# Kernel tuning notes

Hardware: AMD Instinct MI355X
Metric: run time of the kernel (lower is better)

## Reference

```python
import jax, jax.numpy as jnp
import numpy as np

B, T, M, E, H, D = 4, 1024, 1024, 1024, 16, 64
SCALE = D ** (-0.5)


def setup_inputs() -> dict:
    key = jax.random.key(0)
    ks = jax.random.split(key, 8)
    w = 0.02  # weight scale for numerical stability of softmax
    return {
        "x": jax.random.normal(ks[0], (B, T, E), jnp.float32),
        "xl_memory": jax.random.normal(ks[1], (B, M, 2, H * D), jnp.float32),
        "relative_positions": jax.random.normal(ks[2], (H, T, M + T), jnp.float32),
        "Wq": jax.random.normal(ks[3], (E, H * D), jnp.float32) * w,
        "bq": jnp.zeros((H * D,), jnp.float32),
        "Wk": jax.random.normal(ks[4], (E, H * D), jnp.float32) * w,
        "bk": jnp.zeros((H * D,), jnp.float32),
        "Wv": jax.random.normal(ks[5], (E, H * D), jnp.float32) * w,
        "bv": jnp.zeros((H * D,), jnp.float32),
        "Wo": jax.random.normal(ks[6], (H * D, E), jnp.float32) * w,
        "bo": jnp.zeros((E,), jnp.float32),
    }


def reference(x, xl_memory, relative_positions, Wq, bq, Wk, bk, Wv, bv, Wo, bo):
    b, t, _ = x.shape
    q = (x @ Wq + bq) * SCALE                     # [b, t, H*D] (scale applied to queries)
    k = x @ Wk + bk
    v = x @ Wv + bv
    k_xl = xl_memory[:, :, 0]                      # [b, m, H*D]
    v_xl = xl_memory[:, :, 1]
    m = k_xl.shape[1]
    keys = jnp.concatenate((k_xl, k), axis=1)      # [b, j, H*D], j = m + t
    values = jnp.concatenate((v_xl, v), axis=1)
    j = keys.shape[1]

    qh = q.reshape(b, t, H, D).transpose(0, 2, 1, 3)       # b h i d
    kh = keys.reshape(b, j, H, D).transpose(0, 2, 1, 3)    # b h j d
    vh = values.reshape(b, j, H, D).transpose(0, 2, 1, 3)  # b h j d

    qk = jnp.einsum("bhid,bhjd->bhij", qh, kh)
    qk = relative_positions[..., -t:, -j:] + qk
    qk = qk * SCALE                                # second scale, faithful to source
    mask = jnp.triu(jnp.ones((t, j), dtype=bool), j - t + 1)
    qk = jnp.where(mask, -jnp.inf, qk)
    attn = jax.nn.softmax(qk, axis=-1)             # dropout p=0.0 -> identity

    qkv = jnp.einsum("bhij,bhjd->bhid", attn, vh)
    qkv = qkv.transpose(0, 2, 1, 3).reshape(b, t, H * D)
    out = qkv @ Wo + bo

    kv_memories = jnp.stack((keys, values), axis=-2)  # [b, j, 2, H*D]
    kv_to_add_xl = kv_memories[:, -m:]                 # [b, m, 2, H*D]
    return out, kv_to_add_xl
```

## Files before the change

### kernel.cpp

```cpp
#include <hip/hip_runtime.h>
#include <hip/hip_bf16.h>

typedef unsigned short u16;
typedef unsigned int u32;
typedef __attribute__((ext_vector_type(8))) short short8;
typedef __attribute__((ext_vector_type(4))) float f32x4;

#define B_ 4
#define T_ 1024
#define E_ 1024
#define NH 16
#define HD 1024
#define JTOT 2048
#define SCALE 0.125f
#define LOG2E 1.44269504f

__device__ __forceinline__ u16 f2b(float f) {
  u32 x = __float_as_uint(f);
  u32 r = (x + 0x7fffu + ((x >> 16) & 1u)) >> 16;
  return (u16)r;
}
__device__ __forceinline__ u16 f2b_fast(float f) {
  return (u16)((__float_as_uint(f) + 0x8000u) >> 16);
}
__device__ __forceinline__ float b2f(u16 b) {
  return __uint_as_float((u32)b << 16);
}
__device__ __forceinline__ float fexp2(float x) {
  float r;
  asm("v_exp_f32 %0, %1" : "=v"(r) : "v"(x));
  return r;
}
__device__ __forceinline__ u32 cvtpk(float lo, float hi) {
  u32 r;
  asm("v_cvt_pk_bf16_f32 %0, %1, %2" : "=v"(r) : "v"(lo), "v"(hi));
  return r;
}

__device__ __forceinline__ void gload_lds16(const void* g, void* l) {
  __builtin_amdgcn_global_load_lds((const __attribute__((address_space(1))) u32*)g,
                                   (__attribute__((address_space(3))) u32*)l, 16, 0, 0);
}

__device__ __forceinline__ short8 pack8(float4 f0, float4 f1) {
  short8 o;
  o[0] = (short)f2b(f0.x); o[1] = (short)f2b(f0.y);
  o[2] = (short)f2b(f0.z); o[3] = (short)f2b(f0.w);
  o[4] = (short)f2b(f1.x); o[5] = (short)f2b(f1.y);
  o[6] = (short)f2b(f1.z); o[7] = (short)f2b(f1.w);
  return o;
}

__global__ __launch_bounds__(256) void cvt_all(
    const float* __restrict__ x, const float* __restrict__ Wq, const float* __restrict__ Wk,
    const float* __restrict__ Wv, const float* __restrict__ Wo, const float* __restrict__ xl,
    u16* __restrict__ xb, u16* __restrict__ wqkvT, u16* __restrict__ woT,
    u16* __restrict__ kt, u16* __restrict__ vt) {
  int bx = blockIdx.x;
  if (bx < 2048) {
    int i = bx * 256 + threadIdx.x;
    const float4* p = (const float4*)x + (size_t)i * 2;
    ((short8*)xb)[i] = pack8(p[0], p[1]);
  } else if (bx < 3072) {
    __shared__ float tile[64][65];
    int idx = bx - 2048;
    int z = idx >> 8, yy = (idx >> 4) & 15, xx = idx & 15;
    const float* W;
    u16* WT;
    if (z == 0) { W = Wq; WT = wqkvT; }
    else if (z == 1) { W = Wk; WT = wqkvT + (size_t)1024 * 1024; }
    else if (z == 2) { W = Wv; WT = wqkvT + (size_t)2048 * 1024; }
    else { W = Wo; WT = woT; }
    int t = threadIdx.x;
    int r0 = yy * 64, c0 = xx * 64;
#pragma unroll
    for (int i = 0; i < 16; ++i) {
      int r = i * 4 + (t >> 6), c = t & 63;
      tile[r][c] = W[(size_t)(r0 + r) * 1024 + c0 + c];
    }
    __syncthreads();
#pragma unroll
    for (int i = 0; i < 16; ++i) {
      int r = i * 4 + (t >> 6), c = t & 63;
      WT[(size_t)(c0 + r) * 1024 + r0 + c] = f2b(tile[c][r]);
    }
  } else if (bx < 5120) {
    int i = (bx - 3072) * 256 + threadIdx.x;
    int hd8 = i & 127, j = (i >> 7) & 1023, b = i >> 17;
    const float4* p = (const float4*)(xl + ((((size_t)b * 1024 + j) * 2 + 0) * 1024 + (size_t)hd8 * 8));
    short8 o = pack8(p[0], p[1]);
    int h = hd8 >> 3, d0 = (hd8 & 7) * 8;
    int jc = j >> 6, jl = j & 63;
    u16* dst = kt + (((size_t)(b * 16 + h) * 32 + jc) * 4096) + jl * 64 + (d0 ^ ((jl & 7) << 3));
    *(short8*)dst = o;
  } else {
    __shared__ u16 Vl[64 * 72];
    int bxx = bx - 5120;
    int jc = bxx & 15, h = (bxx >> 4) & 15, b = bxx >> 8;
    int t = threadIdx.x;
    int j0 = jc * 64;
#pragma unroll
    for (int it = 0; it < 2; ++it) {
      int p = t + 256 * it;
      int j = p >> 3, d8 = p & 7;
      const float4* src = (const float4*)(xl + ((((size_t)b * 1024 + j0 + j) * 2 + 1) * 1024 + h * 64 + (size_t)d8 * 8));
      *(short8*)&Vl[j * 72 + d8 * 8] = pack8(src[0], src[1]);
    }
    __syncthreads();
#pragma unroll
    for (int it = 0; it < 2; ++it) {
      int p = t + 256 * it;
      int d = p >> 3, j8 = p & 7;
      short8 o;
#pragma unroll
      for (int e = 0; e < 8; ++e) o[e] = (short)Vl[(j8 * 8 + e) * 72 + d];
      u16* dst = vt + (((size_t)(b * 16 + h) * 32 + jc) * 4096) + d * 64 + ((j8 * 8) ^ ((d & 7) << 3));
      *(short8*)dst = o;
    }
  }
}

__global__ __launch_bounds__(256) void gemm_qkv(
    const u16* __restrict__ A, const u16* __restrict__ BT,
    const float* __restrict__ b0, const float* __restrict__ b1, const float* __restrict__ b2,
    u16* __restrict__ qb, u16* __restrict__ kbp, u16* __restrict__ vb) {
  __shared__ __align__(16) u16 As[128 * 32];
  __shared__ __align__(16) u16 Bs[128 * 32];
  const int t = threadIdx.x;
  const int lane = t & 63, wv = t >> 6;
  const int wr = wv >> 1, wc = wv & 1;
  const int xcd = blockIdx.x & 7, loc = blockIdx.x >> 3;
  const int m0 = (loc / 3) * 128;
  const int n0 = (xcd * 3 + loc % 3) * 128;
  const int lr = lane & 15, lg = lane >> 4;

  f32x4 acc[4][4] = {};

  for (int kc = 0; kc < 1024; kc += 32) {
    __syncthreads();
#pragma unroll
    for (int i = 0; i < 2; ++i) {
      int p = t + 256 * i;
      gload_lds16(A + (size_t)(m0 + (p >> 2)) * 1024 + kc + (p & 3) * 8, &As[p * 8]);
    }
#pragma unroll
    for (int i = 0; i < 2; ++i) {
      int p = t + 256 * i;
      gload_lds16(BT + (size_t)(n0 + (p >> 2)) * 1024 + kc + (p & 3) * 8, &Bs[p * 8]);
    }
    __syncthreads();

    short8 af[4], bf[4];
#pragma unroll
    for (int mf = 0; mf < 4; ++mf)
      af[mf] = *(const short8*)&As[(wr * 64 + mf * 16 + lr) * 32 + lg * 8];
#pragma unroll
    for (int nf = 0; nf < 4; ++nf)
      bf[nf] = *(const short8*)&Bs[(wc * 64 + nf * 16 + lr) * 32 + lg * 8];
#pragma unroll
    for (int mf = 0; mf < 4; ++mf)
#pragma unroll
      for (int nf = 0; nf < 4; ++nf)
        acc[mf][nf] = __builtin_amdgcn_mfma_f32_16x16x32_bf16(af[mf], bf[nf], acc[mf][nf], 0, 0, 0);
  }

#pragma unroll
  for (int mf = 0; mf < 4; ++mf) {
#pragma unroll
    for (int nf = 0; nf < 4; ++nf) {
#pragma unroll
      for (int r = 0; r < 4; ++r) {
        int row = m0 + wr * 64 + mf * 16 + lg * 4 + r;
        int col = n0 + wc * 64 + nf * 16 + lr;
        float v = acc[mf][nf][r];
        int b = row >> 10, tt = row & 1023;
        if (col < 1024) {
          qb[(size_t)row * HD + col] = f2b((v + b0[col]) * (SCALE * SCALE * LOG2E));
        } else if (col < 2048) {
          int hd = col - 1024;
          kbp[(size_t)(b * 1024 + tt) * 1024 + hd] = f2b(v + b1[hd]);
        } else {
          int hd = col - 2048;
          vb[(size_t)(b * 1024 + tt) * 1024 + hd] = f2b(v + b2[hd]);
        }
      }
    }
  }
}

__global__ __launch_bounds__(256) void post_gemm(const u16* __restrict__ kbp, const u16* __restrict__ vbp,
                                                 float* __restrict__ kvout, u16* __restrict__ kt,
                                                 u16* __restrict__ vt) {
  int bx = blockIdx.x;
  if (bx < 2048) {
    int i = bx * 256 + threadIdx.x;
    int hd8 = i & 127, tt = (i >> 7) & 1023, b = i >> 17;
    size_t src = ((size_t)(b * 1024 + tt)) * 1024 + (size_t)hd8 * 8;
    short8 k8 = *(const short8*)&kbp[src];
    short8 v8 = *(const short8*)&vbp[src];
    float4 k0, k1, v0, v1;
#pragma unroll
    for (int e = 0; e < 4; ++e) {
      ((float*)&k0)[e] = b2f((u16)k8[e]); ((float*)&k1)[e] = b2f((u16)k8[e + 4]);
      ((float*)&v0)[e] = b2f((u16)v8[e]); ((float*)&v1)[e] = b2f((u16)v8[e + 4]);
    }
    float* kdst = kvout + (((size_t)(b * 1024 + tt) * 2 + 0) * 1024) + hd8 * 8;
    float* vdst = kvout + (((size_t)(b * 1024 + tt) * 2 + 1) * 1024) + hd8 * 8;
    ((float4*)kdst)[0] = k0; ((float4*)kdst)[1] = k1;
    ((float4*)vdst)[0] = v0; ((float4*)vdst)[1] = v1;
    int h = hd8 >> 3, d0 = (hd8 & 7) * 8;
    int jc = 16 + (tt >> 6), jl = tt & 63;
    u16* ktdst = kt + (((size_t)(b * 16 + h) * 32 + jc) * 4096) + jl * 64 + (d0 ^ ((jl & 7) << 3));
    *(short8*)ktdst = k8;
  } else {
    __shared__ u16 Vl[64 * 72];
    int bxx = bx - 2048;
    int jcl = bxx & 15, h = (bxx >> 4) & 15, b = bxx >> 8;
    int jc = 16 + jcl;
    int t = threadIdx.x;
    int t0 = jcl * 64;
#pragma unroll
    for (int it = 0; it < 2; ++it) {
      int p = t + 256 * it;
      int j = p >> 3, d8 = p & 7;
      *(short8*)&Vl[j * 72 + d8 * 8] =
          *(const short8*)&vbp[((size_t)b * 1024 + t0 + j) * 1024 + h * 64 + d8 * 8];
    }
    __syncthreads();
#pragma unroll
    for (int it = 0; it < 2; ++it) {
      int p = t + 256 * it;
      int d = p >> 3, j8 = p & 7;
      short8 o;
#pragma unroll
      for (int e = 0; e < 8; ++e) o[e] = (short)Vl[(j8 * 8 + e) * 72 + d];
      u16* dst = vt + (((size_t)(b * 16 + h) * 32 + jc) * 4096) + d * 64 + ((j8 * 8) ^ ((d & 7) << 3));
      *(short8*)dst = o;
    }
  }
}

__global__ __launch_bounds__(256) void gemm_out(
    const u16* __restrict__ A, const u16* __restrict__ BT,
    const float* __restrict__ bias, float* __restrict__ outf) {
  __shared__ __align__(16) u16 As[64 * 32];
  __shared__ __align__(16) u16 Bs[128 * 32];
  const int t = threadIdx.x;
  const int lane = t & 63, wv = t >> 6;
  const int wr = wv >> 1, wc = wv & 1;
  const int m0 = (blockIdx.x >> 3) * 64;
  const int n0 = (blockIdx.x & 7) * 128;
  const int lr = lane & 15, lg = lane >> 4;

  f32x4 acc[2][4] = {};

  for (int kc = 0; kc < 1024; kc += 32) {
    __syncthreads();
    gload_lds16(A + (size_t)(m0 + (t >> 2)) * 1024 + kc + (t & 3) * 8, &As[t * 8]);
#pragma unroll
    for (int i = 0; i < 2; ++i) {
      int p = t + 256 * i;
      gload_lds16(BT + (size_t)(n0 + (p >> 2)) * 1024 + kc + (p & 3) * 8, &Bs[p * 8]);
    }
    __syncthreads();

    short8 af[2], bf[4];
#pragma unroll
    for (int mf = 0; mf < 2; ++mf)
      af[mf] = *(const short8*)&As[(wr * 32 + mf * 16 + lr) * 32 + lg * 8];
#pragma unroll
    for (int nf = 0; nf < 4; ++nf)
      bf[nf] = *(const short8*)&Bs[(wc * 64 + nf * 16 + lr) * 32 + lg * 8];
#pragma unroll
    for (int mf = 0; mf < 2; ++mf)
#pragma unroll
      for (int nf = 0; nf < 4; ++nf)
        acc[mf][nf] = __builtin_amdgcn_mfma_f32_16x16x32_bf16(af[mf], bf[nf], acc[mf][nf], 0, 0, 0);
  }

#pragma unroll
  for (int mf = 0; mf < 2; ++mf)
#pragma unroll
    for (int nf = 0; nf < 4; ++nf)
#pragma unroll
      for (int r = 0; r < 4; ++r) {
        int row = m0 + wr * 32 + mf * 16 + lg * 4 + r;
        int col = n0 + wc * 64 + nf * 16 + lr;
        outf[(size_t)row * E_ + col] = acc[mf][nf][r] + bias[col];
      }
}

__global__ __launch_bounds__(256) void attn_kernel(
    const u16* __restrict__ qb, const u16* __restrict__ kt, const u16* __restrict__ vt,
    const float* __restrict__ rel, u16* __restrict__ aout) {
  __shared__ __align__(16) u16 Ks[2][4096];
  __shared__ __align__(16) u16 Vs[2][4096];
  __shared__ __align__(16) u16 Pl[4096];
  const int bx = blockIdx.x;
  const int xcd = bx & 7, s = bx >> 3;
  const int b = s & 3, key = (s >> 2) * 8 + xcd;
  const int h = key & 15, qt = key >> 4;
  const int i0 = qt * 64;
  const int t = threadIdx.x, lane = t & 63, w = t >> 6;
  const int lr = lane & 15, lg = lane >> 4;
  const int swz = (lr & 7) << 3;
  const float RC = SCALE * LOG2E;

  const u16* ktb = kt + (size_t)(b * 16 + h) * 32 * 4096;
  const u16* vtb = vt + (size_t)(b * 16 + h) * 32 * 4096;
  const float* relrow = rel + (size_t)h * T_ * JTOT + (size_t)(i0 + w * 16 + lr) * JTOT + lg * 4;
  const int nch = qt + 17;

  short8 qf[2];
#pragma unroll
  for (int kc = 0; kc < 2; ++kc)
    qf[kc] = *(const short8*)&qb[(size_t)(b * T_ + i0 + w * 16 + lr) * HD + h * 64 + kc * 32 + lg * 8];

  short8 vf5;
#pragma unroll
  for (int e = 0; e < 8; ++e) vf5[e] = (lr == 0) ? (short)0x3f80 : (short)0;

  auto stage = [&](int buf, int jc2) {
    const u16* ksrc = ktb + (size_t)jc2 * 4096;
    const u16* vsrc = vtb + (size_t)jc2 * 4096;
    gload_lds16(ksrc + t * 8, &Ks[buf][t * 8]);
    gload_lds16(ksrc + (t + 256) * 8, &Ks[buf][(t + 256) * 8]);
    gload_lds16(vsrc + t * 8, &Vs[buf][t * 8]);
    gload_lds16(vsrc + (t + 256) * 8, &Vs[buf][(t + 256) * 8]);
  };

  auto loadrel = [&](int j0, float4 (&rlf)[4]) {
#pragma unroll
    for (int nf = 0; nf < 4; ++nf)
      rlf[nf] = *(const float4*)(relrow + j0 + nf * 16);
  };

  float4 rlA[4], rlB[4];
  stage(0, 0);
  __builtin_amdgcn_sched_barrier(0);
  loadrel(0, rlA);
  loadrel(64, rlB);

  f32x4 o[4] = {};
  f32x4 o5 = {};
  float mrow = -__builtin_inff();

  int cur = 0;
  auto chunkfn = [&](int jc, float4 (&rlu)[4]) {
    asm volatile("s_waitcnt vmcnt(4)" ::: "memory");
    __builtin_amdgcn_sched_barrier(0);
    asm volatile("s_barrier" ::: "memory");
    if (jc + 1 < nch) stage(cur ^ 1, jc + 1);
    __builtin_amdgcn_sched_barrier(0);

    f32x4 s4[4] = {};
#pragma unroll
    for (int nf = 0; nf < 4; ++nf)
#pragma unroll
      for (int kc = 0; kc < 2; ++kc) {
        short8 kf = *(const short8*)&Ks[cur][(nf * 16 + lr) * 64 + ((kc * 32 + lg * 8) ^ swz)];
        s4[nf] = __builtin_amdgcn_mfma_f32_16x16x32_bf16(kf, qf[kc], s4[nf], 0, 0, 0);
      }

    float p[4][4], lmax = -__builtin_inff();
    const bool domask = (jc == qt + 16);
#pragma unroll
    for (int nf = 0; nf < 4; ++nf)
#pragma unroll
      for (int r = 0; r < 4; ++r) {
        float v = fmaf(((const float*)&rlu[nf])[r], RC, s4[nf][r]);
        if (domask && (nf * 16 + lg * 4 + r) > (w * 16 + lr)) v = -__builtin_inff();
        p[nf][r] = v;
        lmax = fmaxf(lmax, v);
      }
    if (jc + 2 < nch) loadrel((jc + 2) * 64, rlu);

    const bool dores = !__all(lmax - mrow <= 11.0f);
    if (dores) {
      float ch = fmaxf(lmax, __shfl_xor(lmax, 16, 64));
      ch = fmaxf(ch, __shfl_xor(ch, 32, 64));
      float nm = fmaxf(mrow, ch);
      float sc = fexp2(mrow - nm);
      mrow = nm;
      float sco[4];
#pragma unroll
      for (int r = 0; r < 4; ++r) sco[r] = __shfl(sc, lg * 4 + r, 64);
#pragma unroll
      for (int nf = 0; nf < 4; ++nf)
#pragma unroll
        for (int r = 0; r < 4; ++r) o[nf][r] *= sco[r];
#pragma unroll
      for (int r = 0; r < 4; ++r) o5[r] *= sco[r];
    }

    {
      u32* plrow = (u32*)&Pl[(w * 16 + lr) * 64];
#pragma unroll
      for (int nf = 0; nf < 4; ++nf) {
        float e0 = fexp2(p[nf][0] - mrow), e1 = fexp2(p[nf][1] - mrow);
        float e2 = fexp2(p[nf][2] - mrow), e3 = fexp2(p[nf][3] - mrow);
        u32 w0 = cvtpk(e0, e1), w1 = cvtpk(e2, e3);
        plrow[((nf * 16 + lg * 4 + 0) ^ swz) >> 1] = w0;
        plrow[((nf * 16 + lg * 4 + 2) ^ swz) >> 1] = w1;
      }
    }

#pragma unroll
    for (int kc = 0; kc < 2; ++kc) {
      short8 pa = *(const short8*)&Pl[(w * 16 + lr) * 64 + ((kc * 32 + lg * 8) ^ swz)];
#pragma unroll
      for (int nf = 0; nf < 4; ++nf) {
        short8 vf = *(const short8*)&Vs[cur][(nf * 16 + lr) * 64 + ((kc * 32 + lg * 8) ^ swz)];
        o[nf] = __builtin_amdgcn_mfma_f32_16x16x32_bf16(pa, vf, o[nf], 0, 0, 0);
      }
      o5 = __builtin_amdgcn_mfma_f32_16x16x32_bf16(pa, vf5, o5, 0, 0, 0);
    }
    cur ^= 1;
  };

  int jc = 0;
  for (; jc + 1 < nch; jc += 2) {
    chunkfn(jc, rlA);
    chunkfn(jc + 1, rlB);
  }
  if (jc < nch) chunkfn(jc, rlA);

  float inv[4];
#pragma unroll
  for (int r = 0; r < 4; ++r)
    inv[r] = 1.0f / __shfl(o5[r], lane & 48, 64);
#pragma unroll
  for (int nf = 0; nf < 4; ++nf)
#pragma unroll
    for (int r = 0; r < 4; ++r) {
      int i = i0 + w * 16 + lg * 4 + r, d = nf * 16 + lr;
      aout[(size_t)(b * T_ + i) * HD + h * 64 + d] = f2b_fast(o[nf][r] * inv[r]);
    }
}

extern "C" void kernel_launch(void* const* d_in, const int* in_sizes, int n_in,
                              void* d_out, int out_size, void* d_ws, size_t ws_size,
                              hipStream_t stream) {
  const float* x  = (const float*)d_in[0];
  const float* xl = (const float*)d_in[1];
  const float* rel = (const float*)d_in[2];
  const float* Wq = (const float*)d_in[3];
  const float* bq = (const float*)d_in[4];
  const float* Wk = (const float*)d_in[5];
  const float* bk = (const float*)d_in[6];
  const float* Wv = (const float*)d_in[7];
  const float* bv = (const float*)d_in[8];
  const float* Wo = (const float*)d_in[9];
  const float* bo = (const float*)d_in[10];

  float* out = (float*)d_out;
  float* kvout = out + (size_t)B_ * T_ * E_;

  char* ws = (char*)d_ws;
  u16* xb    = (u16*)ws; ws += (size_t)4096 * 1024 * 2;
  u16* wqkvT = (u16*)ws; ws += (size_t)3072 * 1024 * 2;
  u16* woT   = (u16*)ws; ws += (size_t)1024 * 1024 * 2;
  u16* qbuf  = (u16*)ws; ws += (size_t)4096 * 1024 * 2;
  u16* kt    = (u16*)ws; ws += (size_t)B_ * NH * 32 * 4096 * 2;
  u16* vt    = (u16*)ws; ws += (size_t)B_ * NH * 32 * 4096 * 2;
  u16* vbn   = (u16*)ws; ws += (size_t)4096 * 1024 * 2;
  u16* kbp   = (u16*)ws; ws += (size_t)4096 * 1024 * 2;
  u16* aout  = (u16*)ws; ws += (size_t)4096 * 1024 * 2;

  cvt_all<<<6144, 256, 0, stream>>>(x, Wq, Wk, Wv, Wo, xl, xb, wqkvT, woT, kt, vt);
  gemm_qkv<<<768, 256, 0, stream>>>(xb, wqkvT, bq, bk, bv, qbuf, kbp, vbn);
  post_gemm<<<3072, 256, 0, stream>>>(kbp, vbn, kvout, kt, vt);
  attn_kernel<<<1024, 256, 0, stream>>>(qbuf, kt, vt, rel, aout);
  gemm_out<<<512, 256, 0, stream>>>(aout, woT, bo, out);
}
```

Baseline: 203.2 us.

## Single-buffer K tile in LDS and compute softmax row sums with shuffles

K is now single-buffered in LDS. The next chunk's K/V prefetch is issued after the QK^T MFMAs, with an extra barrier, so that LDS usage drops and more occupancy is possible. The row sum of probabilities now comes from shuffle reductions of fp32 exponentials instead of an extra MFMA against a ones-column vector, which removes one MFMA per k-step and the o5 accumulator registers. The cost is less overlap between the K load and compute and a second barrier per chunk. The normalizer now uses unrounded fp32 sums rather than the bf16 P values used in the PV product.

Measured after the change: 209.8 us. 1.03x slower.

```diff
diff --git a/kernel.cpp b/kernel.cpp
--- a/kernel.cpp
+++ b/kernel.cpp
@@ -293,7 +293,7 @@
 __global__ __launch_bounds__(256) void attn_kernel(
     const u16* __restrict__ qb, const u16* __restrict__ kt, const u16* __restrict__ vt,
     const float* __restrict__ rel, u16* __restrict__ aout) {
-  __shared__ __align__(16) u16 Ks[2][4096];
+  __shared__ __align__(16) u16 Ks[4096];
   __shared__ __align__(16) u16 Vs[2][4096];
   __shared__ __align__(16) u16 Pl[4096];
   const int bx = blockIdx.x;
@@ -316,17 +316,13 @@
   for (int kc = 0; kc < 2; ++kc)
     qf[kc] = *(const short8*)&qb[(size_t)(b * T_ + i0 + w * 16 + lr) * HD + h * 64 + kc * 32 + lg * 8];
 
-  short8 vf5;
-#pragma unroll
-  for (int e = 0; e < 8; ++e) vf5[e] = (lr == 0) ? (short)0x3f80 : (short)0;
-
-  auto stage = [&](int buf, int jc2) {
+  auto stageKV = [&](int vbuf, int jc2) {
     const u16* ksrc = ktb + (size_t)jc2 * 4096;
     const u16* vsrc = vtb + (size_t)jc2 * 4096;
-    gload_lds16(ksrc + t * 8, &Ks[buf][t * 8]);
-    gload_lds16(ksrc + (t + 256) * 8, &Ks[buf][(t + 256) * 8]);
-    gload_lds16(vsrc + t * 8, &Vs[buf][t * 8]);
-    gload_lds16(vsrc + (t + 256) * 8, &Vs[buf][(t + 256) * 8]);
+    gload_lds16(ksrc + t * 8, &Ks[t * 8]);
+    gload_lds16(ksrc + (t + 256) * 8, &Ks[(t + 256) * 8]);
+    gload_lds16(vsrc + t * 8, &Vs[vbuf][t * 8]);
+    gload_lds16(vsrc + (t + 256) * 8, &Vs[vbuf][(t + 256) * 8]);
   };
 
   auto loadrel = [&](int j0, float4 (&rlf)[4]) {
@@ -336,13 +332,13 @@
   };
 
   float4 rlA[4], rlB[4];
-  stage(0, 0);
+  stageKV(0, 0);
   __builtin_amdgcn_sched_barrier(0);
   loadrel(0, rlA);
   loadrel(64, rlB);
 
   f32x4 o[4] = {};
-  f32x4 o5 = {};
+  float lsum = 0.f;
   float mrow = -__builtin_inff();
 
   int cur = 0;
@@ -350,17 +346,19 @@
     asm volatile("s_waitcnt vmcnt(4)" ::: "memory");
     __builtin_amdgcn_sched_barrier(0);
     asm volatile("s_barrier" ::: "memory");
-    if (jc + 1 < nch) stage(cur ^ 1, jc + 1);
+
+    f32x4 s4[4] = {};
+#pragma unroll
+    for (int nf = 0; nf < 4; ++nf)
+#pragma unroll
+      for (int kc = 0; kc < 2; ++kc) {
+        short8 kf = *(const short8*)&Ks[(nf * 16 + lr) * 64 + ((kc * 32 + lg * 8) ^ swz)];
+        s4[nf] = __builtin_amdgcn_mfma_f32_16x16x32_bf16(kf, qf[kc], s4[nf], 0, 0, 0);
+      }
+
+    asm volatile("s_barrier" ::: "memory");
+    if (jc + 1 < nch) stageKV(cur ^ 1, jc + 1);
     __builtin_amdgcn_sched_barrier(0);
-
-    f32x4 s4[4] = {};
-#pragma unroll
-    for (int nf = 0; nf < 4; ++nf)
-#pragma unroll
-      for (int kc = 0; kc < 2; ++kc) {
-        short8 kf = *(const short8*)&Ks[cur][(nf * 16 + lr) * 64 + ((kc * 32 + lg * 8) ^ swz)];
-        s4[nf] = __builtin_amdgcn_mfma_f32_16x16x32_bf16(kf, qf[kc], s4[nf], 0, 0, 0);
-      }
 
     float p[4][4], lmax = -__builtin_inff();
     const bool domask = (jc == qt + 16);
@@ -382,6 +380,7 @@
       float nm = fmaxf(mrow, ch);
       float sc = fexp2(mrow - nm);
       mrow = nm;
+      lsum *= sc;
       float sco[4];
 #pragma unroll
       for (int r = 0; r < 4; ++r) sco[r] = __shfl(sc, lg * 4 + r, 64);
@@ -389,21 +388,24 @@
       for (int nf = 0; nf < 4; ++nf)
 #pragma unroll
         for (int r = 0; r < 4; ++r) o[nf][r] *= sco[r];
-#pragma unroll
-      for (int r = 0; r < 4; ++r) o5[r] *= sco[r];
-    }
-
+    }
+
+    float rs = 0.f;
     {
       u32* plrow = (u32*)&Pl[(w * 16 + lr) * 64];
 #pragma unroll
       for (int nf = 0; nf < 4; ++nf) {
         float e0 = fexp2(p[nf][0] - mrow), e1 = fexp2(p[nf][1] - mrow);
         float e2 = fexp2(p[nf][2] - mrow), e3 = fexp2(p[nf][3] - mrow);
+        rs += (e0 + e1) + (e2 + e3);
         u32 w0 = cvtpk(e0, e1), w1 = cvtpk(e2, e3);
         plrow[((nf * 16 + lg * 4 + 0) ^ swz) >> 1] = w0;
         plrow[((nf * 16 + lg * 4 + 2) ^ swz) >> 1] = w1;
       }
     }
+    rs += __shfl_xor(rs, 16, 64);
+    rs += __shfl_xor(rs, 32, 64);
+    lsum += rs;
 
 #pragma unroll
     for (int kc = 0; kc < 2; ++kc) {
@@ -413,7 +415,6 @@
         short8 vf = *(const short8*)&Vs[cur][(nf * 16 + lr) * 64 + ((kc * 32 + lg * 8) ^ swz)];
         o[nf] = __builtin_amdgcn_mfma_f32_16x16x32_bf16(pa, vf, o[nf], 0, 0, 0);
       }
-      o5 = __builtin_amdgcn_mfma_f32_16x16x32_bf16(pa, vf5, o5, 0, 0, 0);
     }
     cur ^= 1;
   };
@@ -428,7 +429,7 @@
   float inv[4];
 #pragma unroll
   for (int r = 0; r < 4; ++r)
-    inv[r] = 1.0f / __shfl(o5[r], lane & 48, 64);
+    inv[r] = 1.0f / __shfl(lsum, lg * 4 + r, 64);
 #pragma unroll
   for (int nf = 0; nf < 4; ++nf)
 #pragma unroll
```
